# Kernel tuning notes

Hardware: AMD Instinct MI355X
Metric: run time of the kernel (lower is better)

The kernel has to match this reference:

```python
import jax, jax.numpy as jnp
import numpy as np

B, T_HIST, D, H, STEPS = 2048, 15, 64, 128, 20
MAX_STEPS = 48           # max adaptive steps per unit time interval
DT0, RTOL, ATOL = 0.1, 1e-3, 1e-6
SAFETY, FMIN, FMAX = 0.9, 0.2, 10.0

# Tsit5 (Tsitouras 2011) tableau
A21 = 0.161
A31, A32 = -0.008480655492356989, 0.335480655492357
A41, A42, A43 = 2.8971530571054935, -6.359448489975075, 4.3622954328695815
A51, A52, A53, A54 = 5.325864828439257, -11.748883564062828, 7.4955393428898365, -0.09249506636175525
A61, A62, A63, A64, A65 = 5.86145544294642, -12.92096931784711, 8.159367898576159, -0.071584973281401, -0.028269050394068383
B1, B2, B3, B4, B5, B6 = 0.09646076681806523, 0.01, 0.4798896504144996, 1.379008574103742, -3.290069515436081, 2.324710524099774
E1, E2, E3, E4, E5, E6, E7 = (-0.00178001105222577714, -0.0008164344596567469, 0.007880878010261995,
                              -0.1447110071732629, 0.5823571654525552, -0.45808210592918697, 0.015151515151515152)


def _mlp(y, W1, b1, W2, b2, W3, b3):
    h = jax.nn.softplus(y @ W1.T + b1)
    h = jax.nn.softplus(h @ W2.T + b2)
    return h @ W3.T + b3


def _solve(y0, W1, b1, W2, b2, W3, b3, steps):
    f = lambda y: _mlp(y, W1, b1, W2, b2, W3, b3)  # batched vector field [B,D]->[B,D]
    Bn = y0.shape[0]

    def segment(carry, t1):
        y, dt = carry
        t = jnp.full((Bn,), t1 - 1.0, y0.dtype)
        done = jnp.zeros((Bn,), bool)

        def body(state, _):
            t, y, dt, done = state
            dt_c = jnp.minimum(dt, t1 - t)          # clip to segment end
            h = dt_c[:, None]
            k1 = f(y)
            k2 = f(y + h * (A21 * k1))
            k3 = f(y + h * (A31 * k1 + A32 * k2))
            k4 = f(y + h * (A41 * k1 + A42 * k2 + A43 * k3))
            k5 = f(y + h * (A51 * k1 + A52 * k2 + A53 * k3 + A54 * k4))
            k6 = f(y + h * (A61 * k1 + A62 * k2 + A63 * k3 + A64 * k4 + A65 * k5))
            y5 = y + h * (B1 * k1 + B2 * k2 + B3 * k3 + B4 * k4 + B5 * k5 + B6 * k6)
            k7 = f(y5)
            err = h * (E1 * k1 + E2 * k2 + E3 * k3 + E4 * k4 + E5 * k5 + E6 * k6 + E7 * k7)
            scale = ATOL + RTOL * jnp.maximum(jnp.abs(y), jnp.abs(y5))
            err_norm = jnp.sqrt(jnp.mean((err / scale) ** 2, axis=-1))  # [B]
            accept = (err_norm <= 1.0) & (~done)
            factor = jnp.clip(SAFETY * jnp.maximum(err_norm, 1e-10) ** (-0.2), FMIN, FMAX)
            t_new = jnp.where(accept, t + dt_c, t)
            y_new = jnp.where(accept[:, None], y5, y)
            dt_new = jnp.where(done, dt, dt_c * factor)
            done_new = done | (t_new >= t1 - 1e-8)
            return (t_new, y_new, dt_new, done_new), None

        (t, y, dt, done), _ = jax.lax.scan(jax.checkpoint(body), (t, y, dt, done), None, length=MAX_STEPS)
        return (y, dt), y

    ts1 = jnp.arange(1, steps + 1, dtype=y0.dtype)
    dt0 = jnp.full((Bn,), DT0, y0.dtype)
    (_, _), ys = jax.lax.scan(segment, (y0, dt0), ts1)  # ys: [steps, B, D]
    return jnp.transpose(ys, (1, 0, 2))                  # [B, steps, D]


def setup_inputs() -> dict:
    key = jax.random.key(0)
    ks = jax.random.split(key, 7)
    history = jax.random.normal(ks[0], (B, T_HIST, D), jnp.float32)
    # small-scale init keeps the vector field mild so adaptive steps converge
    W1 = jax.random.normal(ks[1], (H, D), jnp.float32) * (0.5 / np.sqrt(D))
    b1 = jax.random.normal(ks[2], (H,), jnp.float32) * 0.05
    W2 = jax.random.normal(ks[3], (H, H), jnp.float32) * (0.5 / np.sqrt(H))
    b2 = jax.random.normal(ks[4], (H,), jnp.float32) * 0.05
    W3 = jax.random.normal(ks[5], (D, H), jnp.float32) * (0.1 / np.sqrt(H))
    b3 = jax.random.normal(ks[6], (D,), jnp.float32) * 0.05
    return {"history": history, "W1": W1, "b1": b1, "W2": W2, "b2": b2, "W3": W3, "b3": b3, "steps": STEPS}


def reference(history, W1, b1, W2, b2, W3, b3, steps):
    y0 = history[:, -1]  # NeuralODE uses only the last history state
    return _solve(y0, W1, b1, W2, b2, W3, b3, steps)
```

## Files before the change

### kernel.cpp

```cpp
#include <hip/hip_runtime.h>
#include <math.h>

#define NB    2048
#define NSEG  20
#define MAXIT 48

typedef __attribute__((ext_vector_type(8))) short bf8_t;
typedef __attribute__((ext_vector_type(4))) float f32x4;

#define cA21 ((float)0.161)
#define cA31 ((float)-0.008480655492356989)
#define cA32 ((float)0.335480655492357)
#define cA41 ((float)2.8971530571054935)
#define cA42 ((float)-6.359448489975075)
#define cA43 ((float)4.3622954328695815)
#define cA51 ((float)5.325864828439257)
#define cA52 ((float)-11.748883564062828)
#define cA53 ((float)7.4955393428898365)
#define cA54 ((float)-0.09249506636175525)
#define cA61 ((float)5.86145544294642)
#define cA62 ((float)-12.92096931784711)
#define cA63 ((float)8.159367898576159)
#define cA64 ((float)-0.071584973281401)
#define cA65 ((float)-0.028269050394068383)
#define cB1  ((float)0.09646076681806523)
#define cB2  ((float)0.01)
#define cB3  ((float)0.4798896504144996)
#define cB4  ((float)1.379008574103742)
#define cB5  ((float)-3.290069515436081)
#define cB6  ((float)2.324710524099774)
#define cE1  ((float)-0.001780011052225777)
#define cE2  ((float)-0.0008164344596567469)
#define cE3  ((float)0.007880878010261995)
#define cE4  ((float)-0.1447110071732629)
#define cE5  ((float)0.5823571654525552)
#define cE6  ((float)-0.45808210592918697)
#define cE7  ((float)0.015151515151515152)

__device__ __forceinline__ void split2(float x, short &hi, short &lo) {
    unsigned u = __float_as_uint(x);
    hi = (short)(u >> 16);
    float r = x - __uint_as_float(u & 0xFFFF0000u);
    lo = (short)(__float_as_uint(r) >> 16);
}

__device__ __forceinline__ float softplus_f(float x) {
    float t = exp2f(-fabsf(x) * 1.442695040888963f);
    return fmaxf(x, 0.0f) + log2f(1.0f + t) * 0.6931471805599453f;
}

__device__ __forceinline__ unsigned pk(short a, short b) {
    return ((unsigned)(unsigned short)a) | (((unsigned)(unsigned short)b) << 16);
}

__global__ __launch_bounds__(512)
void ode_kernel(const float* __restrict__ history,
                const float* __restrict__ W1, const float* __restrict__ b1,
                const float* __restrict__ W2, const float* __restrict__ b2,
                const float* __restrict__ W3, const float* __restrict__ b3,
                float* __restrict__ out)
{
    __shared__ alignas(16) short argH[2 * 544], argL[2 * 544];
    __shared__ alignas(16) short h1H[4 * 544], h1L[4 * 544];
    __shared__ alignas(16) short h2H[4 * 544], h2L[4 * 544];
    __shared__ alignas(16) float kcur[8 * 68];
    __shared__ int doneF[8];

    const int tid  = threadIdx.x;
    const int wave = tid >> 6, lane = tid & 63;
    const int quad = lane >> 4, col = lane & 15;
    const int jb   = 16 * wave + 4 * quad;

    bf8_t A1h[2], A1l[2], A2h[4], A2l[4], A3h[4], A3l[4];
#pragma unroll
    for (int c = 0; c < 2; ++c) {
        const float* p = W1 + (size_t)(16 * wave + col) * 64 + 32 * c + 8 * quad;
        bf8_t h, l;
#pragma unroll
        for (int j = 0; j < 8; ++j) { short hs, ls; split2(p[j], hs, ls); h[j] = hs; l[j] = ls; }
        A1h[c] = h; A1l[c] = l;
    }
#pragma unroll
    for (int c = 0; c < 4; ++c) {
        const float* p = W2 + (size_t)(16 * wave + col) * 128 + 32 * c + 8 * quad;
        bf8_t h, l;
#pragma unroll
        for (int j = 0; j < 8; ++j) { short hs, ls; split2(p[j], hs, ls); h[j] = hs; l[j] = ls; }
        A2h[c] = h; A2l[c] = l;
    }
    f32x4 b3f = {0.f, 0.f, 0.f, 0.f};
    if (wave < 4) {
#pragma unroll
        for (int c = 0; c < 4; ++c) {
            const float* p = W3 + (size_t)(16 * wave + col) * 128 + 32 * c + 8 * quad;
            bf8_t h, l;
#pragma unroll
            for (int j = 0; j < 8; ++j) { short hs, ls; split2(p[j], hs, ls); h[j] = hs; l[j] = ls; }
            A3h[c] = h; A3l[c] = l;
        }
        b3f = *(const f32x4*)(b3 + jb);
    } else {
        bf8_t z = {0, 0, 0, 0, 0, 0, 0, 0};
#pragma unroll
        for (int c = 0; c < 4; ++c) { A3h[c] = z; A3l[c] = z; }
    }
    const f32x4 b1f = *(const f32x4*)(b1 + jb);
    const f32x4 b2f = *(const f32x4*)(b2 + jb);

    const int aidx = (lane >> 5) * 544 + ((lane >> 3) & 3) * 136 + wave * 8 + (lane & 7);
    const int elem = blockIdx.x * 8 + wave;

    auto gemm = [&](const bf8_t* Ah, const bf8_t* Al, const short* BH, const short* BL,
                    int nch) -> f32x4 {
        f32x4 acc = {0.f, 0.f, 0.f, 0.f};
#pragma unroll
        for (int c = 0; c < nch; ++c) {
            const int off = c * 544 + quad * 136 + col * 8;
            bf8_t bh = *(const bf8_t*)(BH + off);
            bf8_t bl = *(const bf8_t*)(BL + off);
            acc = __builtin_amdgcn_mfma_f32_16x16x32_bf16(Al[c], bh, acc, 0, 0, 0);
            acc = __builtin_amdgcn_mfma_f32_16x16x32_bf16(Ah[c], bl, acc, 0, 0, 0);
            acc = __builtin_amdgcn_mfma_f32_16x16x32_bf16(Ah[c], bh, acc, 0, 0, 0);
        }
        return acc;
    };

    auto epi = [&](f32x4 acc, f32x4 bias, short* H, short* L) {
        if (col < 8) {
            const int idx = (jb >> 5) * 544 + ((jb >> 3) & 3) * 136 + col * 8 + (jb & 7);
            short hh[4], ll[4];
#pragma unroll
            for (int r = 0; r < 4; ++r) {
                float v = softplus_f(acc[r] + bias[r]);
                split2(v, hh[r], ll[r]);
            }
            *(uint2*)(H + idx) = make_uint2(pk(hh[0], hh[1]), pk(hh[2], hh[3]));
            *(uint2*)(L + idx) = make_uint2(pk(ll[0], ll[1]), pk(ll[2], ll[3]));
        }
    };

    auto eval = [&]() {
        __syncthreads();
        f32x4 a1 = gemm(A1h, A1l, argH, argL, 2);
        epi(a1, b1f, h1H, h1L);
        __syncthreads();
        f32x4 a2 = gemm(A2h, A2l, h1H, h1L, 4);
        epi(a2, b2f, h2H, h2L);
        __syncthreads();
        if (wave < 4) {
            f32x4 a3 = gemm(A3h, A3l, h2H, h2L, 4);
            if (col < 8) {
                f32x4 kv;
#pragma unroll
                for (int r = 0; r < 4; ++r) kv[r] = a3[r] + b3f[r];
                *(f32x4*)(kcur + col * 68 + jb) = kv;
            }
        }
        __syncthreads();
    };

    float y  = history[((size_t)elem * 15 + 14) * 64 + lane];
    float dt = 0.1f;
    float k1, k2, k3, k4, k5, k6;

    {
        short hi, lo; split2(y, hi, lo);
        argH[aidx] = hi; argL[aidx] = lo;
        eval();
        k1 = kcur[wave * 68 + lane];
    }

#pragma unroll 1
    for (int seg = 1; seg <= NSEG; ++seg) {
        const float t1 = (float)seg;
        float t = t1 - 1.0f;
        bool done = false;

#pragma unroll 1
        for (int it = 0; it < MAXIT; ++it) {
            const float dt_c = fminf(dt, t1 - t);
            const float h = dt_c;
            float y5v = 0.f, k7v = 0.f;

#pragma unroll 1
            for (int st = 2; st <= 7; ++st) {
                float sum;
                switch (st) {
                    case 2: sum = cA21 * k1; break;
                    case 3: sum = fmaf(cA31, k1, cA32 * k2); break;
                    case 4: sum = fmaf(cA41, k1, fmaf(cA42, k2, cA43 * k3)); break;
                    case 5: sum = fmaf(cA51, k1, fmaf(cA52, k2, fmaf(cA53, k3, cA54 * k4))); break;
                    case 6: sum = fmaf(cA61, k1, fmaf(cA62, k2, fmaf(cA63, k3, fmaf(cA64, k4, cA65 * k5)))); break;
                    default: sum = fmaf(cB1, k1, fmaf(cB2, k2, fmaf(cB3, k3, fmaf(cB4, k4, fmaf(cB5, k5, cB6 * k6))))); break;
                }
                float arg = fmaf(h, sum, y);
                if (st == 7) y5v = arg;
                short hi, lo; split2(arg, hi, lo);
                argH[aidx] = hi; argL[aidx] = lo;
                eval();
                float kv = kcur[wave * 68 + lane];
                switch (st) {
                    case 2: k2 = kv; break;
                    case 3: k3 = kv; break;
                    case 4: k4 = kv; break;
                    case 5: k5 = kv; break;
                    case 6: k6 = kv; break;
                    default: k7v = kv; break;
                }
            }

            float esum = fmaf(cE1, k1, fmaf(cE2, k2, fmaf(cE3, k3,
                         fmaf(cE4, k4, fmaf(cE5, k5, fmaf(cE6, k6, cE7 * k7v))))));
            float err = h * esum;
            float sc = fmaf(1e-3f, fmaxf(fabsf(y), fabsf(y5v)), 1e-6f);
            float r = err / sc;
            float rr = r * r;
#pragma unroll
            for (int off = 32; off > 0; off >>= 1) rr += __shfl_xor(rr, off, 64);
            float en = sqrtf(rr * (1.0f / 64.0f));

            bool accept = (en <= 1.0f) && !done;
            float fac = 0.9f * exp2f(-0.2f * log2f(fmaxf(en, 1e-10f)));
            fac = fminf(fmaxf(fac, 0.2f), 10.0f);

            if (accept) { t += dt_c; y = y5v; k1 = k7v; }
            if (!done) dt = dt_c * fac;
            done = done || (t >= t1 - 1e-8f);

            if (lane == 0) doneF[wave] = done ? 1 : 0;
            __syncthreads();
            bool all = true;
#pragma unroll
            for (int e2 = 0; e2 < 8; ++e2) all = all && (doneF[e2] != 0);
            if (all) break;
        }

        out[((size_t)elem * NSEG + (seg - 1)) * 64 + lane] = y;
    }
}

extern "C" void kernel_launch(void* const* d_in, const int* in_sizes, int n_in,
                              void* d_out, int out_size, void* d_ws, size_t ws_size,
                              hipStream_t stream) {
    const float* history = (const float*)d_in[0];
    const float* W1 = (const float*)d_in[1];
    const float* b1 = (const float*)d_in[2];
    const float* W2 = (const float*)d_in[3];
    const float* b2 = (const float*)d_in[4];
    const float* W3 = (const float*)d_in[5];
    const float* b3 = (const float*)d_in[6];
    float* out = (float*)d_out;

    ode_kernel<<<dim3(NB / 8), dim3(512), 0, stream>>>(history, W1, b1, W2, b2, W3, b3, out);
}
```

Measured before the change: 335.3 us.

## Compact LDS layout, split MFMA accumulators, spread softplus epilogue across all lanes via DPP

Shrinks the shared-memory operand layout from 16 padded columns to 8, which are the only batch elements used. The three-way bf16 split MFMAs now accumulate into independent registers and are summed at the end, which breaks the serial dependency chain between MFMA instructions. The epilogue uses a DPP row-shift so all 16 column lanes each handle two outputs, instead of half the lanes doing four softplus evaluations. This should cut epilogue latency and MFMA stalls, at the cost of extra registers and a changed summation order.

```diff
diff --git a/kernel.cpp b/kernel.cpp
--- a/kernel.cpp
+++ b/kernel.cpp
@@ -4,6 +4,8 @@
 #define NB    2048
 #define NSEG  20
 #define MAXIT 48
+#define CH    288
+#define BLKS  72
 
 typedef __attribute__((ext_vector_type(8))) short bf8_t;
 typedef __attribute__((ext_vector_type(4))) float f32x4;
@@ -53,6 +55,12 @@
     return ((unsigned)(unsigned short)a) | (((unsigned)(unsigned short)b) << 16);
 }
 
+__device__ __forceinline__ float dpp_sel_shr8(float own, float up) {
+    int r = __builtin_amdgcn_update_dpp(__float_as_int(own), __float_as_int(up),
+                                        0x118, 0xF, 0xC, false);
+    return __int_as_float(r);
+}
+
 __global__ __launch_bounds__(512)
 void ode_kernel(const float* __restrict__ history,
                 const float* __restrict__ W1, const float* __restrict__ b1,
@@ -60,9 +68,9 @@
                 const float* __restrict__ W3, const float* __restrict__ b3,
                 float* __restrict__ out)
 {
-    __shared__ alignas(16) short argH[2 * 544], argL[2 * 544];
-    __shared__ alignas(16) short h1H[4 * 544], h1L[4 * 544];
-    __shared__ alignas(16) short h2H[4 * 544], h2L[4 * 544];
+    __shared__ alignas(16) short argH[2 * CH], argL[2 * CH];
+    __shared__ alignas(16) short h1H[4 * CH], h1L[4 * CH];
+    __shared__ alignas(16) short h2H[4 * CH], h2L[4 * CH];
     __shared__ alignas(16) float kcur[8 * 68];
     __shared__ int doneF[8];
 
@@ -107,36 +115,46 @@
     const f32x4 b1f = *(const f32x4*)(b1 + jb);
     const f32x4 b2f = *(const f32x4*)(b2 + jb);
 
-    const int aidx = (lane >> 5) * 544 + ((lane >> 3) & 3) * 136 + wave * 8 + (lane & 7);
+    const int aidx = (lane >> 5) * CH + ((lane >> 3) & 3) * BLKS + wave * 8 + (lane & 7);
     const int elem = blockIdx.x * 8 + wave;
+
+    const int esel  = (lane >> 3) & 1;
+    const int eelem = lane & 7;
+    const int ejrow = 4 * quad + 2 * esel;
+
+    const int boff = quad * BLKS + (col & 7) * 8;
 
     auto gemm = [&](const bf8_t* Ah, const bf8_t* Al, const short* BH, const short* BL,
                     int nch) -> f32x4 {
-        f32x4 acc = {0.f, 0.f, 0.f, 0.f};
+        f32x4 a0 = {0.f, 0.f, 0.f, 0.f}, a1 = a0, a2 = a0;
 #pragma unroll
         for (int c = 0; c < nch; ++c) {
-            const int off = c * 544 + quad * 136 + col * 8;
+            const int off = c * CH + boff;
             bf8_t bh = *(const bf8_t*)(BH + off);
             bf8_t bl = *(const bf8_t*)(BL + off);
-            acc = __builtin_amdgcn_mfma_f32_16x16x32_bf16(Al[c], bh, acc, 0, 0, 0);
-            acc = __builtin_amdgcn_mfma_f32_16x16x32_bf16(Ah[c], bl, acc, 0, 0, 0);
-            acc = __builtin_amdgcn_mfma_f32_16x16x32_bf16(Ah[c], bh, acc, 0, 0, 0);
-        }
+            a0 = __builtin_amdgcn_mfma_f32_16x16x32_bf16(Ah[c], bh, a0, 0, 0, 0);
+            a1 = __builtin_amdgcn_mfma_f32_16x16x32_bf16(Ah[c], bl, a1, 0, 0, 0);
+            a2 = __builtin_amdgcn_mfma_f32_16x16x32_bf16(Al[c], bh, a2, 0, 0, 0);
+        }
+        f32x4 acc;
+#pragma unroll
+        for (int r = 0; r < 4; ++r) acc[r] = a0[r] + (a1[r] + a2[r]);
         return acc;
     };
 
     auto epi = [&](f32x4 acc, f32x4 bias, short* H, short* L) {
-        if (col < 8) {
-            const int idx = (jb >> 5) * 544 + ((jb >> 3) & 3) * 136 + col * 8 + (jb & 7);
-            short hh[4], ll[4];
-#pragma unroll
-            for (int r = 0; r < 4; ++r) {
-                float v = softplus_f(acc[r] + bias[r]);
-                split2(v, hh[r], ll[r]);
-            }
-            *(uint2*)(H + idx) = make_uint2(pk(hh[0], hh[1]), pk(hh[2], hh[3]));
-            *(uint2*)(L + idx) = make_uint2(pk(ll[0], ll[1]), pk(ll[2], ll[3]));
-        }
+        float v0 = acc[0] + bias[0], v1 = acc[1] + bias[1];
+        float v2 = acc[2] + bias[2], v3 = acc[3] + bias[3];
+        float x0 = dpp_sel_shr8(v0, v2);
+        float x1 = dpp_sel_shr8(v1, v3);
+        float s0 = softplus_f(x0), s1 = softplus_f(x1);
+        short h0, l0, h1, l1;
+        split2(s0, h0, l0);
+        split2(s1, h1, l1);
+        const int j0  = 16 * wave + ejrow;
+        const int idx = (j0 >> 5) * CH + ((j0 >> 3) & 3) * BLKS + eelem * 8 + (j0 & 7);
+        *(unsigned*)(H + idx) = pk(h0, h1);
+        *(unsigned*)(L + idx) = pk(l0, l1);
     };
 
     auto eval = [&]() {
```

Result: faster. 311.5 us (-7.1%).

## Interleave hi/lo bf16 halves into one B operand and fold columns with DPP

Applied to the files above, without the earlier changes.

The activation tiles now store the bf16 high and low halves of each batch element in adjacent N columns of a single shared buffer (columns 0-7 hi, 8-15 lo), so each MFMA chunk needs one B load and two MFMAs (Ah·B, Al·B) instead of two loads and three MFMAs. The hi and lo column contributions are summed with a DPP row-shift-by-8 fold before the bias and softplus. The epilogue is spread across all 16 columns, each lane handling two outputs. This trades the third MFMA and a separate lo buffer for extra DPP adds and slightly more complex indexing, and it keeps the same split-bf16 precision scheme.

```diff
diff --git a/kernel.cpp b/kernel.cpp
--- a/kernel.cpp
+++ b/kernel.cpp
@@ -4,6 +4,8 @@
 #define NB    2048
 #define NSEG  20
 #define MAXIT 48
+#define CH    544
+#define BLKS  136
 
 typedef __attribute__((ext_vector_type(8))) short bf8_t;
 typedef __attribute__((ext_vector_type(4))) float f32x4;
@@ -53,6 +55,12 @@
     return ((unsigned)(unsigned short)a) | (((unsigned)(unsigned short)b) << 16);
 }
 
+__device__ __forceinline__ float fold8(float x) {
+    int r = __builtin_amdgcn_update_dpp(__float_as_int(x), __float_as_int(x),
+                                        0x128, 0xF, 0xF, false);
+    return x + __int_as_float(r);
+}
+
 __global__ __launch_bounds__(512)
 void ode_kernel(const float* __restrict__ history,
                 const float* __restrict__ W1, const float* __restrict__ b1,
@@ -60,9 +68,9 @@
                 const float* __restrict__ W3, const float* __restrict__ b3,
                 float* __restrict__ out)
 {
-    __shared__ alignas(16) short argH[2 * 544], argL[2 * 544];
-    __shared__ alignas(16) short h1H[4 * 544], h1L[4 * 544];
-    __shared__ alignas(16) short h2H[4 * 544], h2L[4 * 544];
+    __shared__ alignas(16) short argB[2 * CH];
+    __shared__ alignas(16) short h1B[4 * CH];
+    __shared__ alignas(16) short h2B[4 * CH];
     __shared__ alignas(16) float kcur[8 * 68];
     __shared__ int doneF[8];
 
@@ -107,54 +115,59 @@
     const f32x4 b1f = *(const f32x4*)(b1 + jb);
     const f32x4 b2f = *(const f32x4*)(b2 + jb);
 
-    const int aidx = (lane >> 5) * 544 + ((lane >> 3) & 3) * 136 + wave * 8 + (lane & 7);
+    const int aidx = (lane >> 5) * CH + ((lane >> 3) & 3) * BLKS + wave * 8 + (lane & 7);
     const int elem = blockIdx.x * 8 + wave;
 
-    auto gemm = [&](const bf8_t* Ah, const bf8_t* Al, const short* BH, const short* BL,
-                    int nch) -> f32x4 {
-        f32x4 acc = {0.f, 0.f, 0.f, 0.f};
+    const int esel  = col >> 3;
+    const int eelem = col & 7;
+    const int j0    = 16 * wave + 4 * quad + 2 * esel;
+    const int epidx = (j0 >> 5) * CH + ((j0 >> 3) & 3) * BLKS + eelem * 8 + (j0 & 7);
+
+    const int boff = quad * BLKS + col * 8;
+
+    auto gemm = [&](const bf8_t* Ah, const bf8_t* Al, const short* Bc, int nch) -> f32x4 {
+        f32x4 a0 = {0.f, 0.f, 0.f, 0.f}, a1 = a0;
 #pragma unroll
         for (int c = 0; c < nch; ++c) {
-            const int off = c * 544 + quad * 136 + col * 8;
-            bf8_t bh = *(const bf8_t*)(BH + off);
-            bf8_t bl = *(const bf8_t*)(BL + off);
-            acc = __builtin_amdgcn_mfma_f32_16x16x32_bf16(Al[c], bh, acc, 0, 0, 0);
-            acc = __builtin_amdgcn_mfma_f32_16x16x32_bf16(Ah[c], bl, acc, 0, 0, 0);
-            acc = __builtin_amdgcn_mfma_f32_16x16x32_bf16(Ah[c], bh, acc, 0, 0, 0);
-        }
-        return acc;
+            bf8_t b = *(const bf8_t*)(Bc + c * CH + boff);
+            a0 = __builtin_amdgcn_mfma_f32_16x16x32_bf16(Ah[c], b, a0, 0, 0, 0);
+            a1 = __builtin_amdgcn_mfma_f32_16x16x32_bf16(Al[c], b, a1, 0, 0, 0);
+        }
+        f32x4 s;
+#pragma unroll
+        for (int r = 0; r < 4; ++r) s[r] = a0[r] + a1[r];
+        return s;
     };
 
-    auto epi = [&](f32x4 acc, f32x4 bias, short* H, short* L) {
-        if (col < 8) {
-            const int idx = (jb >> 5) * 544 + ((jb >> 3) & 3) * 136 + col * 8 + (jb & 7);
-            short hh[4], ll[4];
-#pragma unroll
-            for (int r = 0; r < 4; ++r) {
-                float v = softplus_f(acc[r] + bias[r]);
-                split2(v, hh[r], ll[r]);
-            }
-            *(uint2*)(H + idx) = make_uint2(pk(hh[0], hh[1]), pk(hh[2], hh[3]));
-            *(uint2*)(L + idx) = make_uint2(pk(ll[0], ll[1]), pk(ll[2], ll[3]));
-        }
+    auto epi = [&](f32x4 s, f32x4 bias, short* Bn) {
+        float t0 = fold8(s[0]) + bias[0];
+        float t1 = fold8(s[1]) + bias[1];
+        float t2 = fold8(s[2]) + bias[2];
+        float t3 = fold8(s[3]) + bias[3];
+        float x0 = esel ? t2 : t0;
+        float x1 = esel ? t3 : t1;
+        float p0 = softplus_f(x0), p1 = softplus_f(x1);
+        short h0, l0, h1, l1;
+        split2(p0, h0, l0);
+        split2(p1, h1, l1);
+        *(unsigned*)(Bn + epidx)      = pk(h0, h1);
+        *(unsigned*)(Bn + epidx + 64) = pk(l0, l1);
     };
 
     auto eval = [&]() {
         __syncthreads();
-        f32x4 a1 = gemm(A1h, A1l, argH, argL, 2);
-        epi(a1, b1f, h1H, h1L);
-        __syncthreads();
-        f32x4 a2 = gemm(A2h, A2l, h1H, h1L, 4);
-        epi(a2, b2f, h2H, h2L);
+        f32x4 s1 = gemm(A1h, A1l, argB, 2);
+        epi(s1, b1f, h1B);
+        __syncthreads();
+        f32x4 s2 = gemm(A2h, A2l, h1B, 4);
+        epi(s2, b2f, h2B);
         __syncthreads();
         if (wave < 4) {
-            f32x4 a3 = gemm(A3h, A3l, h2H, h2L, 4);
-            if (col < 8) {
-                f32x4 kv;
-#pragma unroll
-                for (int r = 0; r < 4; ++r) kv[r] = a3[r] + b3f[r];
-                *(f32x4*)(kcur + col * 68 + jb) = kv;
-            }
+            f32x4 s3 = gemm(A3h, A3l, h2B, 4);
+            f32x4 kv;
+#pragma unroll
+            for (int r = 0; r < 4; ++r) kv[r] = fold8(s3[r]) + b3f[r];
+            if (col < 8) *(f32x4*)(kcur + col * 68 + jb) = kv;
         }
         __syncthreads();
     };
@@ -165,7 +178,7 @@
 
     {
         short hi, lo; split2(y, hi, lo);
-        argH[aidx] = hi; argL[aidx] = lo;
+        argB[aidx] = hi; argB[aidx + 64] = lo;
         eval();
         k1 = kcur[wave * 68 + lane];
     }
@@ -196,7 +209,7 @@
                 float arg = fmaf(h, sum, y);
                 if (st == 7) y5v = arg;
                 short hi, lo; split2(arg, hi, lo);
-                argH[aidx] = hi; argL[aidx] = lo;
+                argB[aidx] = hi; argB[aidx + 64] = lo;
                 eval();
                 float kv = kcur[wave * 68 + lane];
                 switch (st) {
```

Result: faster. 283.4 us (-15.5%).

## Repack MLP MFMA work to 4 elements per 256-thread block with K-split folds

Applied to the files above, without the earlier changes.

Shrinks each block from 8 ODE elements on 8 waves to 4 elements on 4 waves, launching twice as many blocks with two blocks per CU. The hi/lo bf16 split is packed into one interleaved shared buffer, and each MFMA multiplies weights against the combined hi/lo operand, dropping from three MFMAs per chunk to two. Partial sums are reduced across lanes with DPP folds. The per-element state is spread over 16 lanes per wave, so the error norm is reduced through shared memory, and the done check becomes a wave vote. The aim is to cut wasted MFMA work (the old 8-column padding and idle W3 waves), cut synchronisation cost, and cut stalls from lockstep adaptive stepping across 8 elements. In exchange it adds more cross-lane folds, an extra barrier per step, and lower per-block reuse of the weights held in registers.

```diff
diff --git a/kernel.cpp b/kernel.cpp
--- a/kernel.cpp
+++ b/kernel.cpp
@@ -4,6 +4,8 @@
 #define NB    2048
 #define NSEG  20
 #define MAXIT 48
+#define CH    288
+#define BLKS  72
 
 typedef __attribute__((ext_vector_type(8))) short bf8_t;
 typedef __attribute__((ext_vector_type(4))) float f32x4;
@@ -49,126 +51,184 @@
     return fmaxf(x, 0.0f) + log2f(1.0f + t) * 0.6931471805599453f;
 }
 
-__device__ __forceinline__ unsigned pk(short a, short b) {
-    return ((unsigned)(unsigned short)a) | (((unsigned)(unsigned short)b) << 16);
-}
-
-__global__ __launch_bounds__(512)
+__device__ __forceinline__ float fold4(float x) {
+    int t1 = __builtin_amdgcn_update_dpp(__float_as_int(x), __float_as_int(x),
+                                         0x124, 0xF, 0x5, false);
+    int t2 = __builtin_amdgcn_update_dpp(t1, __float_as_int(x),
+                                         0x12C, 0xF, 0xA, false);
+    return x + __int_as_float(t2);
+}
+
+__device__ __forceinline__ float fold8(float x) {
+    int r = __builtin_amdgcn_update_dpp(__float_as_int(x), __float_as_int(x),
+                                        0x128, 0xF, 0xF, false);
+    return x + __int_as_float(r);
+}
+
+__global__ __launch_bounds__(256, 2)
 void ode_kernel(const float* __restrict__ history,
                 const float* __restrict__ W1, const float* __restrict__ b1,
                 const float* __restrict__ W2, const float* __restrict__ b2,
                 const float* __restrict__ W3, const float* __restrict__ b3,
                 float* __restrict__ out)
 {
-    __shared__ alignas(16) short argH[2 * 544], argL[2 * 544];
-    __shared__ alignas(16) short h1H[4 * 544], h1L[4 * 544];
-    __shared__ alignas(16) short h2H[4 * 544], h2L[4 * 544];
-    __shared__ alignas(16) float kcur[8 * 68];
-    __shared__ int doneF[8];
+    __shared__ alignas(16) short argB[2 * CH];
+    __shared__ alignas(16) short h1B[4 * CH];
+    __shared__ alignas(16) short h2B[4 * CH];
+    __shared__ float rrP[16];
 
     const int tid  = threadIdx.x;
     const int wave = tid >> 6, lane = tid & 63;
     const int quad = lane >> 4, col = lane & 15;
-    const int jb   = 16 * wave + 4 * quad;
-
-    bf8_t A1h[2], A1l[2], A2h[4], A2l[4], A3h[4], A3l[4];
-#pragma unroll
-    for (int c = 0; c < 2; ++c) {
-        const float* p = W1 + (size_t)(16 * wave + col) * 64 + 32 * c + 8 * quad;
-        bf8_t h, l;
-#pragma unroll
-        for (int j = 0; j < 8; ++j) { short hs, ls; split2(p[j], hs, ls); h[j] = hs; l[j] = ls; }
-        A1h[c] = h; A1l[c] = l;
+    const int rsel = col >> 2, e = col & 3;
+    const int d0   = 16 * wave + 4 * quad + rsel;
+    const size_t elemIdx = (size_t)blockIdx.x * 4 + e;
+
+    bf8_t A1h[2][2], A1l[2][2], A2h[2][4], A2l[2][4], A3h[4], A3l[4];
+#pragma unroll
+    for (int tt = 0; tt < 2; ++tt) {
+        const int row = 16 * (2 * wave + tt) + col;
+#pragma unroll
+        for (int c = 0; c < 2; ++c) {
+            const float* p = W1 + (size_t)row * 64 + 32 * c + 8 * quad;
+            bf8_t h, l;
+#pragma unroll
+            for (int j = 0; j < 8; ++j) { short hs, ls; split2(p[j], hs, ls); h[j] = hs; l[j] = ls; }
+            A1h[tt][c] = h; A1l[tt][c] = l;
+        }
+#pragma unroll
+        for (int c = 0; c < 4; ++c) {
+            const float* p = W2 + (size_t)row * 128 + 32 * c + 8 * quad;
+            bf8_t h, l;
+#pragma unroll
+            for (int j = 0; j < 8; ++j) { short hs, ls; split2(p[j], hs, ls); h[j] = hs; l[j] = ls; }
+            A2h[tt][c] = h; A2l[tt][c] = l;
+        }
     }
-#pragma unroll
-    for (int c = 0; c < 4; ++c) {
-        const float* p = W2 + (size_t)(16 * wave + col) * 128 + 32 * c + 8 * quad;
-        bf8_t h, l;
-#pragma unroll
-        for (int j = 0; j < 8; ++j) { short hs, ls; split2(p[j], hs, ls); h[j] = hs; l[j] = ls; }
-        A2h[c] = h; A2l[c] = l;
-    }
-    f32x4 b3f = {0.f, 0.f, 0.f, 0.f};
-    if (wave < 4) {
+    {
+        const int row = 16 * wave + col;
 #pragma unroll
         for (int c = 0; c < 4; ++c) {
-            const float* p = W3 + (size_t)(16 * wave + col) * 128 + 32 * c + 8 * quad;
+            const float* p = W3 + (size_t)row * 128 + 32 * c + 8 * quad;
             bf8_t h, l;
 #pragma unroll
             for (int j = 0; j < 8; ++j) { short hs, ls; split2(p[j], hs, ls); h[j] = hs; l[j] = ls; }
             A3h[c] = h; A3l[c] = l;
         }
-        b3f = *(const f32x4*)(b3 + jb);
-    } else {
-        bf8_t z = {0, 0, 0, 0, 0, 0, 0, 0};
-#pragma unroll
-        for (int c = 0; c < 4; ++c) { A3h[c] = z; A3l[c] = z; }
     }
-    const f32x4 b1f = *(const f32x4*)(b1 + jb);
-    const f32x4 b2f = *(const f32x4*)(b2 + jb);
-
-    const int aidx = (lane >> 5) * 544 + ((lane >> 3) & 3) * 136 + wave * 8 + (lane & 7);
-    const int elem = blockIdx.x * 8 + wave;
-
-    auto gemm = [&](const bf8_t* Ah, const bf8_t* Al, const short* BH, const short* BL,
-                    int nch) -> f32x4 {
-        f32x4 acc = {0.f, 0.f, 0.f, 0.f};
-#pragma unroll
-        for (int c = 0; c < nch; ++c) {
-            const int off = c * 544 + quad * 136 + col * 8;
-            bf8_t bh = *(const bf8_t*)(BH + off);
-            bf8_t bl = *(const bf8_t*)(BL + off);
-            acc = __builtin_amdgcn_mfma_f32_16x16x32_bf16(Al[c], bh, acc, 0, 0, 0);
-            acc = __builtin_amdgcn_mfma_f32_16x16x32_bf16(Ah[c], bl, acc, 0, 0, 0);
-            acc = __builtin_amdgcn_mfma_f32_16x16x32_bf16(Ah[c], bh, acc, 0, 0, 0);
-        }
-        return acc;
+    f32x4 b1f[2], b2f[2];
+#pragma unroll
+    for (int tt = 0; tt < 2; ++tt) {
+        b1f[tt] = *(const f32x4*)(b1 + 16 * (2 * wave + tt) + 4 * quad);
+        b2f[tt] = *(const f32x4*)(b2 + 16 * (2 * wave + tt) + 4 * quad);
+    }
+    const f32x4 b3f = *(const f32x4*)(b3 + 16 * wave + 4 * quad);
+
+    const int boff = quad * BLKS + (col & 7) * 8;
+    const int aidx = (d0 >> 5) * CH + ((d0 >> 3) & 3) * BLKS + e * 8 + (d0 & 7);
+
+    auto epiT = [&](f32x4 s, const f32x4& bias, int rowT, short* Bn) {
+        float f0 = fold4(s[0]) + bias[0];
+        float f1 = fold4(s[1]) + bias[1];
+        float f2 = fold4(s[2]) + bias[2];
+        float f3 = fold4(s[3]) + bias[3];
+        float vlo = (col & 4) ? f1 : f0;
+        float vhi = (col & 4) ? f3 : f2;
+        float v   = (col & 8) ? vhi : vlo;
+        float p = softplus_f(v);
+        short hh, ll; split2(p, hh, ll);
+        const int j   = rowT + 4 * quad + rsel;
+        const int idx = (j >> 5) * CH + ((j >> 3) & 3) * BLKS + e * 8 + (j & 7);
+        Bn[idx]      = hh;
+        Bn[idx + 32] = ll;
     };
 
-    auto epi = [&](f32x4 acc, f32x4 bias, short* H, short* L) {
-        if (col < 8) {
-            const int idx = (jb >> 5) * 544 + ((jb >> 3) & 3) * 136 + col * 8 + (jb & 7);
-            short hh[4], ll[4];
+    auto eval = [&]() -> float {
+        __syncthreads();
+        {
+            f32x4 z = {0.f, 0.f, 0.f, 0.f};
+            f32x4 a0h = z, a0l = z, a1h = z, a1l = z;
+#pragma unroll
+            for (int c = 0; c < 2; ++c) {
+                bf8_t b = *(const bf8_t*)(argB + c * CH + boff);
+                a0h = __builtin_amdgcn_mfma_f32_16x16x32_bf16(A1h[0][c], b, a0h, 0, 0, 0);
+                a0l = __builtin_amdgcn_mfma_f32_16x16x32_bf16(A1l[0][c], b, a0l, 0, 0, 0);
+                a1h = __builtin_amdgcn_mfma_f32_16x16x32_bf16(A1h[1][c], b, a1h, 0, 0, 0);
+                a1l = __builtin_amdgcn_mfma_f32_16x16x32_bf16(A1l[1][c], b, a1l, 0, 0, 0);
+            }
+            f32x4 s0, s1;
+#pragma unroll
+            for (int r = 0; r < 4; ++r) { s0[r] = a0h[r] + a0l[r]; s1[r] = a1h[r] + a1l[r]; }
+            epiT(s0, b1f[0], 32 * wave,      h1B);
+            epiT(s1, b1f[1], 32 * wave + 16, h1B);
+        }
+        __syncthreads();
+        {
+            f32x4 z = {0.f, 0.f, 0.f, 0.f};
+            f32x4 aA[2][2] = {{z, z}, {z, z}}, aB[2][2] = {{z, z}, {z, z}};
+#pragma unroll
+            for (int c = 0; c < 2; ++c) {
+                bf8_t b = *(const bf8_t*)(h1B + c * CH + boff);
+                aA[0][0] = __builtin_amdgcn_mfma_f32_16x16x32_bf16(A2h[0][c], b, aA[0][0], 0, 0, 0);
+                aA[0][1] = __builtin_amdgcn_mfma_f32_16x16x32_bf16(A2l[0][c], b, aA[0][1], 0, 0, 0);
+                aA[1][0] = __builtin_amdgcn_mfma_f32_16x16x32_bf16(A2h[1][c], b, aA[1][0], 0, 0, 0);
+                aA[1][1] = __builtin_amdgcn_mfma_f32_16x16x32_bf16(A2l[1][c], b, aA[1][1], 0, 0, 0);
+            }
+#pragma unroll
+            for (int c = 2; c < 4; ++c) {
+                bf8_t b = *(const bf8_t*)(h1B + c * CH + boff);
+                aB[0][0] = __builtin_amdgcn_mfma_f32_16x16x32_bf16(A2h[0][c], b, aB[0][0], 0, 0, 0);
+                aB[0][1] = __builtin_amdgcn_mfma_f32_16x16x32_bf16(A2l[0][c], b, aB[0][1], 0, 0, 0);
+                aB[1][0] = __builtin_amdgcn_mfma_f32_16x16x32_bf16(A2h[1][c], b, aB[1][0], 0, 0, 0);
+                aB[1][1] = __builtin_amdgcn_mfma_f32_16x16x32_bf16(A2l[1][c], b, aB[1][1], 0, 0, 0);
+            }
+            f32x4 s0, s1;
 #pragma unroll
             for (int r = 0; r < 4; ++r) {
-                float v = softplus_f(acc[r] + bias[r]);
-                split2(v, hh[r], ll[r]);
-            }
-            *(uint2*)(H + idx) = make_uint2(pk(hh[0], hh[1]), pk(hh[2], hh[3]));
-            *(uint2*)(L + idx) = make_uint2(pk(ll[0], ll[1]), pk(ll[2], ll[3]));
+                s0[r] = (aA[0][0][r] + aA[0][1][r]) + (aB[0][0][r] + aB[0][1][r]);
+                s1[r] = (aA[1][0][r] + aA[1][1][r]) + (aB[1][0][r] + aB[1][1][r]);
+            }
+            epiT(s0, b2f[0], 32 * wave,      h2B);
+            epiT(s1, b2f[1], 32 * wave + 16, h2B);
+        }
+        __syncthreads();
+        {
+            f32x4 z = {0.f, 0.f, 0.f, 0.f};
+            f32x4 pAh = z, pAl = z, pBh = z, pBl = z;
+#pragma unroll
+            for (int c = 0; c < 2; ++c) {
+                bf8_t b = *(const bf8_t*)(h2B + c * CH + boff);
+                pAh = __builtin_amdgcn_mfma_f32_16x16x32_bf16(A3h[c], b, pAh, 0, 0, 0);
+                pAl = __builtin_amdgcn_mfma_f32_16x16x32_bf16(A3l[c], b, pAl, 0, 0, 0);
+            }
+#pragma unroll
+            for (int c = 2; c < 4; ++c) {
+                bf8_t b = *(const bf8_t*)(h2B + c * CH + boff);
+                pBh = __builtin_amdgcn_mfma_f32_16x16x32_bf16(A3h[c], b, pBh, 0, 0, 0);
+                pBl = __builtin_amdgcn_mfma_f32_16x16x32_bf16(A3l[c], b, pBl, 0, 0, 0);
+            }
+            float f0 = fold4((pAh[0] + pAl[0]) + (pBh[0] + pBl[0])) + b3f[0];
+            float f1 = fold4((pAh[1] + pAl[1]) + (pBh[1] + pBl[1])) + b3f[1];
+            float f2 = fold4((pAh[2] + pAl[2]) + (pBh[2] + pBl[2])) + b3f[2];
+            float f3 = fold4((pAh[3] + pAl[3]) + (pBh[3] + pBl[3])) + b3f[3];
+            float vlo = (col & 4) ? f1 : f0;
+            float vhi = (col & 4) ? f3 : f2;
+            return (col & 8) ? vhi : vlo;
         }
     };
 
-    auto eval = [&]() {
-        __syncthreads();
-        f32x4 a1 = gemm(A1h, A1l, argH, argL, 2);
-        epi(a1, b1f, h1H, h1L);
-        __syncthreads();
-        f32x4 a2 = gemm(A2h, A2l, h1H, h1L, 4);
-        epi(a2, b2f, h2H, h2L);
-        __syncthreads();
-        if (wave < 4) {
-            f32x4 a3 = gemm(A3h, A3l, h2H, h2L, 4);
-            if (col < 8) {
-                f32x4 kv;
-#pragma unroll
-                for (int r = 0; r < 4; ++r) kv[r] = a3[r] + b3f[r];
-                *(f32x4*)(kcur + col * 68 + jb) = kv;
-            }
-        }
-        __syncthreads();
+    auto argw = [&](float a) {
+        short hh, ll; split2(a, hh, ll);
+        argB[aidx]      = hh;
+        argB[aidx + 32] = ll;
     };
 
-    float y  = history[((size_t)elem * 15 + 14) * 64 + lane];
+    float y  = history[(elemIdx * 15 + 14) * 64 + d0];
     float dt = 0.1f;
     float k1, k2, k3, k4, k5, k6;
 
-    {
-        short hi, lo; split2(y, hi, lo);
-        argH[aidx] = hi; argL[aidx] = lo;
-        eval();
-        k1 = kcur[wave * 68 + lane];
-    }
+    argw(y);
+    k1 = eval();
 
 #pragma unroll 1
     for (int seg = 1; seg <= NSEG; ++seg) {
@@ -195,10 +255,8 @@
                 }
                 float arg = fmaf(h, sum, y);
                 if (st == 7) y5v = arg;
-                short hi, lo; split2(arg, hi, lo);
-                argH[aidx] = hi; argL[aidx] = lo;
-                eval();
-                float kv = kcur[wave * 68 + lane];
+                argw(arg);
+                float kv = eval();
                 switch (st) {
                     case 2: k2 = kv; break;
                     case 3: k3 = kv; break;
@@ -215,9 +273,14 @@
             float sc = fmaf(1e-3f, fmaxf(fabsf(y), fabsf(y5v)), 1e-6f);
             float r = err / sc;
             float rr = r * r;
-#pragma unroll
-            for (int off = 32; off > 0; off >>= 1) rr += __shfl_xor(rr, off, 64);
-            float en = sqrtf(rr * (1.0f / 64.0f));
+            rr += __shfl_xor(rr, 16, 64);
+            rr += __shfl_xor(rr, 32, 64);
+            rr = fold4(rr);
+            rr = fold8(rr);
+            if (lane < 4) rrP[wave * 4 + lane] = rr;
+            __syncthreads();
+            float rs = ((rrP[e] + rrP[4 + e]) + rrP[8 + e]) + rrP[12 + e];
+            float en = sqrtf(rs * (1.0f / 64.0f));
 
             bool accept = (en <= 1.0f) && !done;
             float fac = 0.9f * exp2f(-0.2f * log2f(fmaxf(en, 1e-10f)));
@@ -226,16 +289,10 @@
             if (accept) { t += dt_c; y = y5v; k1 = k7v; }
             if (!done) dt = dt_c * fac;
             done = done || (t >= t1 - 1e-8f);
-
-            if (lane == 0) doneF[wave] = done ? 1 : 0;
-            __syncthreads();
-            bool all = true;
-#pragma unroll
-            for (int e2 = 0; e2 < 8; ++e2) all = all && (doneF[e2] != 0);
-            if (all) break;
-        }
-
-        out[((size_t)elem * NSEG + (seg - 1)) * 64 + lane] = y;
+            if (__all(done)) break;
+        }
+
+        out[(elemIdx * NSEG + (seg - 1)) * 64 + d0] = y;
     }
 }
 
@@ -251,5 +308,5 @@
     const float* b3 = (const float*)d_in[6];
     float* out = (float*)d_out;
 
-    ode_kernel<<<dim3(NB / 8), dim3(512), 0, stream>>>(history, W1, b1, W2, b2, W3, b3, out);
-}
+    ode_kernel<<<dim3(NB / 4), dim3(256), 0, stream>>>(history, W1, b1, W2, b2, W3, b3, out);
+}
```

Result: faster. 312.2 us (-6.9%).
